# Performance work log

Measured on AMD Instinct MI355X. Metric: run time of the kernel, lower is better.

Reference implementation:

```python
import jax, jax.numpy as jnp
import numpy as np

B, L, D, M = 8, 2048, 512, 256
D2, H = 2 * D, 4 * D  # attention d_model, FFN hidden
EPS = 1e-6


def setup_inputs() -> dict:
    key = jax.random.key(0)
    ks = jax.random.split(key, 16)
    s2 = 1.0 / np.sqrt(D2)
    sD = 1.0 / np.sqrt(D)
    sH = 1.0 / np.sqrt(H)
    f32 = jnp.float32
    return {
        "zr": jax.random.normal(ks[0], (B, L, D), f32),
        "zi": jax.random.normal(ks[1], (B, L, D), f32),
        "Wq": jax.random.normal(ks[2], (D2, D2), f32) * s2,
        "Wk": jax.random.normal(ks[3], (D2, D2), f32) * s2,
        "Wv": jax.random.normal(ks[4], (D2, D2), f32) * s2,
        "Wo": jax.random.normal(ks[5], (D2, D2), f32) * s2,
        "Wf": jax.random.normal(ks[6], (M, D2), f32),  # trainable random features (std normal, FAVOR+)
        "b_attn": jnp.zeros((D,), f32),
        "W1r": jax.random.normal(ks[7], (D, H), f32) * sD,
        "W1i": jax.random.normal(ks[8], (D, H), f32) * sD,
        "b1r": jnp.zeros((H,), f32),
        "b1i": jnp.zeros((H,), f32),
        "W2r": jax.random.normal(ks[9], (H, D), f32) * sH,
        "W2i": jax.random.normal(ks[10], (H, D), f32) * sH,
        "b2r": jnp.zeros((D,), f32),
        "b2i": jnp.zeros((D,), f32),
        "b_ffn": jnp.zeros((D,), f32),
    }


def modrelu(xr, xi, b):
    # ModReLU: relu(|z| + b) * z / |z|, per-channel bias b
    mag = jnp.sqrt(xr * xr + xi * xi + EPS)
    s = jax.nn.relu(mag + b) / mag
    return xr * s, xi * s


def _block(zr, zi, Wq, Wk, Wv, Wo, Wf, b_attn,
           W1r, W1i, b1r, b1i, W2r, W2i, b2r, b2i, b_ffn):
    # --- kernelized linear attention on real/imag concat [B,L,2D] ---
    x = jnp.concatenate([zr, zi], axis=-1)
    scl = D2 ** -0.25
    q = (x @ Wq) * scl
    k = (x @ Wk) * scl
    v = x @ Wv
    # FAVOR+ positive features: phi(u) = exp(Wf u - |u|^2/2) / sqrt(m)
    pq = q @ Wf.T - 0.5 * jnp.sum(q * q, axis=-1, keepdims=True)  # [B,L,M]
    pk = k @ Wf.T - 0.5 * jnp.sum(k * k, axis=-1, keepdims=True)
    phi_q = jnp.exp(pq - jax.lax.stop_gradient(jnp.max(pq, axis=-1, keepdims=True))) / np.sqrt(M)
    phi_k = jnp.exp(pk - jax.lax.stop_gradient(jnp.max(pk))) / np.sqrt(M)
    kv = jnp.einsum('blm,bld->bmd', phi_k, v)              # [B,M,2D]
    den = jnp.einsum('blm,bm->bl', phi_q, phi_k.sum(axis=1))  # [B,L]
    y = jnp.einsum('blm,bmd->bld', phi_q, kv) / (den[..., None] + EPS)
    y = y @ Wo
    yr, yi = y[..., :D], y[..., D:]
    # Add & Norm (ModReLU)
    zr, zi = modrelu(zr + yr, zi + yi, b_attn)
    # --- complex FFN: complex Linear -> CReLU -> complex Linear ---
    hr = zr @ W1r - zi @ W1i + b1r
    hi = zr @ W1i + zi @ W1r + b1i
    hr = jax.nn.relu(hr)
    hi = jax.nn.relu(hi)
    fr = hr @ W2r - hi @ W2i + b2r
    fi = hr @ W2i + hi @ W2r + b2i
    # Add & Norm (ModReLU)
    zr, zi = modrelu(zr + fr, zi + fi, b_ffn)
    return jnp.stack([zr, zi], axis=-1)  # [B,L,D,2]


def reference(zr, zi, Wq, Wk, Wv, Wo, Wf, b_attn,
              W1r, W1i, b1r, b1i, W2r, W2i, b2r, b2i, b_ffn):
    return _block(zr, zi, Wq, Wk, Wv, Wo, Wf, b_attn,
                  W1r, W1i, b1r, b1i, W2r, W2i, b2r, b2i, b_ffn)
```

## Files before the change

### kernel.cpp

```cpp
#include <hip/hip_runtime.h>
#include <math.h>

#define B_ 8
#define L_ 2048
#define D_ 512
#define M_ 256
#define D2_ 1024
#define H_ 2048
#define N_ 16384
#define EPS_ 1e-6f

typedef __attribute__((ext_vector_type(8))) short bf16x8;
typedef __attribute__((ext_vector_type(4))) float f32x4;
typedef unsigned short ushort_t;
typedef unsigned int uint_t;

#define WAITCNT_VM8 0x0F78
#define WAITCNT_VM6 0x0F76
#define WAITCNT_VM4 0x0F74
#define WAITCNT_VM0 0x0F70

__device__ __forceinline__ ushort_t f2bf(float f) {
    uint_t u = __float_as_uint(f);
    u += 0x7FFFu + ((u >> 16) & 1u);
    return (ushort_t)(u >> 16);
}
__device__ __forceinline__ float bf2f(ushort_t u) {
    return __uint_as_float(((uint_t)u) << 16);
}
__device__ __forceinline__ void gload_lds16(const void* g, void* l) {
    __builtin_amdgcn_global_load_lds(
        (const __attribute__((address_space(1))) void*)g,
        (__attribute__((address_space(3))) void*)l, 16, 0, 0);
}

__global__ __launch_bounds__(256)
void gemm_mfma(const ushort_t* __restrict__ A, const ushort_t* __restrict__ Bm,
               void* __restrict__ Cp, int K, int lda, int ldb, int ldc,
               long long sA, long long sB, long long sC,
               int epi, float alpha, const float* __restrict__ aux,
               int auxStride, const float* __restrict__ bias, int obf)
{
    __shared__ ushort_t As[4][128 * 32];
    __shared__ ushort_t Bs[4][128 * 32];

    const int bz = blockIdx.z;
    A  += (long long)bz * sA;
    Bm += (long long)bz * sB;
    const int row0 = blockIdx.y * 128;
    const int col0 = blockIdx.x * 128;

    const int tid  = threadIdx.x;
    const int lane = tid & 63;
    const int wave = tid >> 6;
    const int wr = wave >> 1, wc = wave & 1;

    const int srow = tid >> 2;
    const int skol = (((tid & 3) ^ ((tid >> 3) & 3)) * 8);

    f32x4 acc[4][4];
    #pragma unroll
    for (int i = 0; i < 4; ++i)
        #pragma unroll
        for (int j = 0; j < 4; ++j)
            acc[i][j] = (f32x4){0.f, 0.f, 0.f, 0.f};

    const int fr = lane & 15;
    const int fq = lane >> 4;
    const int koff = ((fq ^ ((fr >> 1) & 3))) * 8;

    const int nT = K >> 5;

    auto issue = [&](int t) {
        const int buf = t & 3;
        const int k0 = t << 5;
        gload_lds16(A + (long long)(row0 + srow) * lda + k0 + skol,
                    &As[buf][(wave * 16) * 32]);
        gload_lds16(A + (long long)(row0 + 64 + srow) * lda + k0 + skol,
                    &As[buf][(64 + wave * 16) * 32]);
        gload_lds16(Bm + (long long)(col0 + srow) * ldb + k0 + skol,
                    &Bs[buf][(wave * 16) * 32]);
        gload_lds16(Bm + (long long)(col0 + 64 + srow) * ldb + k0 + skol,
                    &Bs[buf][(64 + wave * 16) * 32]);
    };

    issue(0);
    if (nT > 1) issue(1);
    for (int t = 0; t < nT; ++t) {
        if (t + 2 < nT) {
            issue(t + 2);
            __builtin_amdgcn_s_waitcnt(WAITCNT_VM8);
        } else if (t + 1 < nT) {
            __builtin_amdgcn_s_waitcnt(WAITCNT_VM4);
        } else {
            __builtin_amdgcn_s_waitcnt(WAITCNT_VM0);
        }
        __builtin_amdgcn_s_barrier();

        const int cur = t & 3;
        bf16x8 a[4], b[4];
        #pragma unroll
        for (int i = 0; i < 4; ++i)
            a[i] = *(const bf16x8*)&As[cur][(wr * 64 + i * 16 + fr) * 32 + koff];
        #pragma unroll
        for (int j = 0; j < 4; ++j)
            b[j] = *(const bf16x8*)&Bs[cur][(wc * 64 + j * 16 + fr) * 32 + koff];
        #pragma unroll
        for (int i = 0; i < 4; ++i)
            #pragma unroll
            for (int j = 0; j < 4; ++j)
                acc[i][j] = __builtin_amdgcn_mfma_f32_16x16x32_bf16(
                    a[i], b[j], acc[i][j], 0, 0, 0);
    }

    const int gr0 = row0 + wr * 64;
    const int gc0 = col0 + wc * 64;
    #pragma unroll
    for (int i = 0; i < 4; ++i) {
        #pragma unroll
        for (int r = 0; r < 4; ++r) {
            const int row = gr0 + i * 16 + fq * 4 + r;
            float raux = 0.f;
            if (epi == 1 || epi == 2) raux = aux[(long long)bz * auxStride + row];
            #pragma unroll
            for (int j = 0; j < 4; ++j) {
                const int col = gc0 + j * 16 + fr;
                float v = acc[i][j][r];
                if (epi == 0)      v *= alpha;
                else if (epi == 1) v -= 0.5f * raux;
                else if (epi == 2) v = v / (raux + EPS_);
                else if (epi == 5) v -= 0.5f * aux[(long long)bz * auxStride + col];
                else if (epi == 3) { v += bias[col]; v = v > 0.f ? v : 0.f; }
                else if (epi == 4) v += bias[col];
                const long long off = (long long)bz * sC + (long long)row * ldc + col;
                if (obf) ((ushort_t*)Cp)[off] = f2bf(v);
                else     ((float*)Cp)[off] = v;
            }
        }
    }
}

__global__ __launch_bounds__(512, 2)
void gemm256(const ushort_t* __restrict__ A, const ushort_t* __restrict__ Bm,
             void* __restrict__ Cp, int K, int lda, int ldb, int ldc,
             long long sA, long long sB, long long sC,
             int epi, float alpha, const float* __restrict__ aux,
             int auxStride, const float* __restrict__ bias, int obf)
{
    __shared__ ushort_t As[2][256 * 64];
    __shared__ ushort_t Bs[2][256 * 64];

    const int bz = blockIdx.z;
    A  += (long long)bz * sA;
    Bm += (long long)bz * sB;
    const int row0 = blockIdx.y * 256;
    const int col0 = blockIdx.x * 256;

    const int tid  = threadIdx.x;
    const int lane = tid & 63;
    const int wave = tid >> 6;
    const int wr   = wave >> 2;
    const int wcn  = wave & 3;

    const int rloc  = tid >> 3;
    const int csrc8 = (((tid & 7) ^ (rloc & 7)) << 3);

    const int fr = lane & 15;
    const int fq = lane >> 4;
    const int sw = fr & 7;
    const int c0off = ((fq ^ sw) << 3);
    const int c1off = (((4 | fq) ^ sw) << 3);

    const int nT = K >> 6;

    f32x4 acc[8][4];
    #pragma unroll
    for (int i = 0; i < 8; ++i)
        #pragma unroll
        for (int j = 0; j < 4; ++j)
            acc[i][j] = (f32x4){0.f, 0.f, 0.f, 0.f};

    bf16x8 a[4][2];
    bf16x8 b[4][2];

    auto stage = [&](int bufS, int tS, int half) {
        const int k0 = tS << 6;
        const int rh = (half >= 2) ? 1 : 0;
        const bool isA = (half == 0 || half == 3);
        const ushort_t* g = isA
            ? A  + (long long)(row0 + rh * 128 + rloc) * lda + k0 + csrc8
            : Bm + (long long)(col0 + rh * 128 + rloc) * ldb + k0 + csrc8;
        const long long gstep = 64LL * (isA ? lda : ldb);
        ushort_t* l = (isA ? &As[bufS][0] : &Bs[bufS][0])
                      + (rh * 128 + wave * 8) * 64;
        gload_lds16(g, l);
        gload_lds16(g + gstep, l + 64 * 64);
    };

    auto ldsA = [&](int buf, int mh, int i, int koff) -> bf16x8 {
        return *(const bf16x8*)
            &As[buf][(wr * 128 + mh * 64 + i * 16 + fr) * 64 + koff];
    };
    auto ldsB = [&](int buf, int j, int koff) -> bf16x8 {
        return *(const bf16x8*)
            &Bs[buf][(wcn * 64 + j * 16 + fr) * 64 + koff];
    };

    stage(0, 0, 0); stage(0, 0, 1); stage(0, 0, 2); stage(0, 0, 3);
    stage(1, 1, 0); stage(1, 1, 1); stage(1, 1, 2);
    __builtin_amdgcn_s_waitcnt(WAITCNT_VM6);
    __builtin_amdgcn_s_barrier();

    auto tile_body = [&](int t, int buf) {
        #pragma unroll
        for (int i = 0; i < 4; ++i) {
            a[i][0] = ldsA(buf, 0, i, c0off);
            a[i][1] = ldsA(buf, 0, i, c1off);
        }
        #pragma unroll
        for (int j = 0; j < 2; ++j) {
            b[j][0] = ldsB(buf, j, c0off);
            b[j][1] = ldsB(buf, j, c1off);
        }
        if (t + 1 < nT) stage(buf ^ 1, t + 1, 3);
        __builtin_amdgcn_s_barrier();
        asm volatile("s_waitcnt lgkmcnt(0)" ::: "memory");
        __builtin_amdgcn_s_setprio(1);
        #pragma unroll
        for (int i = 0; i < 4; ++i)
            #pragma unroll
            for (int j = 0; j < 2; ++j) {
                acc[i][j] = __builtin_amdgcn_mfma_f32_16x16x32_bf16(
                    a[i][0], b[j][0], acc[i][j], 0, 0, 0);
                acc[i][j] = __builtin_amdgcn_mfma_f32_16x16x32_bf16(
                    a[i][1], b[j][1], acc[i][j], 0, 0, 0);
            }
        __builtin_amdgcn_s_setprio(0);
        __builtin_amdgcn_s_barrier();

        #pragma unroll
        for (int j = 2; j < 4; ++j) {
            b[j][0] = ldsB(buf, j, c0off);
            b[j][1] = ldsB(buf, j, c1off);
        }
        __builtin_amdgcn_s_barrier();
        asm volatile("s_waitcnt lgkmcnt(0)" ::: "memory");
        __builtin_amdgcn_s_setprio(1);
        #pragma unroll
        for (int i = 0; i < 4; ++i)
            #pragma unroll
            for (int j = 2; j < 4; ++j) {
                acc[i][j] = __builtin_amdgcn_mfma_f32_16x16x32_bf16(
                    a[i][0], b[j][0], acc[i][j], 0, 0, 0);
                acc[i][j] = __builtin_amdgcn_mfma_f32_16x16x32_bf16(
                    a[i][1], b[j][1], acc[i][j], 0, 0, 0);
            }
        __builtin_amdgcn_s_setprio(0);
        __builtin_amdgcn_s_barrier();

        #pragma unroll
        for (int i = 0; i < 4; ++i) {
            a[i][0] = ldsA(buf, 1, i, c0off);
            a[i][1] = ldsA(buf, 1, i, c1off);
        }
        if (t + 2 < nT) stage(buf, t + 2, 1);
        __builtin_amdgcn_s_barrier();
        asm volatile("s_waitcnt lgkmcnt(0)" ::: "memory");
        __builtin_amdgcn_s_setprio(1);
        #pragma unroll
        for (int i = 0; i < 4; ++i)
            #pragma unroll
            for (int j = 2; j < 4; ++j) {
                acc[4 + i][j] = __builtin_amdgcn_mfma_f32_16x16x32_bf16(
                    a[i][0], b[j][0], acc[4 + i][j], 0, 0, 0);
                acc[4 + i][j] = __builtin_amdgcn_mfma_f32_16x16x32_bf16(
                    a[i][1], b[j][1], acc[4 + i][j], 0, 0, 0);
            }
        __builtin_amdgcn_s_setprio(0);
        __builtin_amdgcn_s_barrier();

        if (t + 2 < nT) { stage(buf, t + 2, 2); stage(buf, t + 2, 0); }
        __builtin_amdgcn_s_barrier();
        asm volatile("s_waitcnt lgkmcnt(0)" ::: "memory");
        __builtin_amdgcn_s_setprio(1);
        #pragma unroll
        for (int i = 0; i < 4; ++i)
            #pragma unroll
            for (int j = 0; j < 2; ++j) {
                acc[4 + i][j] = __builtin_amdgcn_mfma_f32_16x16x32_bf16(
                    a[i][0], b[j][0], acc[4 + i][j], 0, 0, 0);
                acc[4 + i][j] = __builtin_amdgcn_mfma_f32_16x16x32_bf16(
                    a[i][1], b[j][1], acc[4 + i][j], 0, 0, 0);
            }
        __builtin_amdgcn_s_setprio(0);
        if (t + 2 < nT)      __builtin_amdgcn_s_waitcnt(WAITCNT_VM6);
        else if (t + 1 < nT) __builtin_amdgcn_s_waitcnt(WAITCNT_VM0);
        __builtin_amdgcn_s_barrier();
    };

    for (int t = 0; t < nT; t += 2) {
        tile_body(t, 0);
        tile_body(t + 1, 1);
    }

    const int gr0 = row0 + wr * 128;
    const int gc0 = col0 + wcn * 64;
    #pragma unroll
    for (int i = 0; i < 8; ++i) {
        #pragma unroll
        for (int r = 0; r < 4; ++r) {
            const int row = gr0 + i * 16 + fq * 4 + r;
            float raux = 0.f;
            if (epi == 1 || epi == 2) raux = aux[(long long)bz * auxStride + row];
            #pragma unroll
            for (int j = 0; j < 4; ++j) {
                const int col = gc0 + j * 16 + fr;
                float v = acc[i][j][r];
                if (epi == 0)      v *= alpha;
                else if (epi == 1) v -= 0.5f * raux;
                else if (epi == 2) v = v / (raux + EPS_);
                else if (epi == 5) v -= 0.5f * aux[(long long)bz * auxStride + col];
                else if (epi == 3) { v += bias[col]; v = v > 0.f ? v : 0.f; }
                else if (epi == 4) v += bias[col];
                const long long off = (long long)bz * sC + (long long)row * ldc + col;
                if (obf) ((ushort_t*)Cp)[off] = f2bf(v);
                else     ((float*)Cp)[off] = v;
            }
        }
    }
}


__global__ __launch_bounds__(256)
void transpose_cvt_sq(const float* __restrict__ W, ushort_t* __restrict__ out)
{
    __shared__ float S[32][33];
    const int tx = threadIdx.x & 31, ty = threadIdx.x >> 5;
    const int n0 = blockIdx.x * 32, k0 = blockIdx.y * 32;
    #pragma unroll
    for (int r = 0; r < 4; ++r)
        S[ty + 8 * r][tx] = W[(long long)(k0 + ty + 8 * r) * 1024 + n0 + tx];
    __syncthreads();
    #pragma unroll
    for (int r = 0; r < 4; ++r)
        out[(long long)(n0 + ty + 8 * r) * 1024 + k0 + tx] = f2bf(S[tx][ty + 8 * r]);
}

__global__ __launch_bounds__(256)
void build_wc1T(const float* __restrict__ W1r, const float* __restrict__ W1i,
                ushort_t* __restrict__ out)
{
    __shared__ float S[32][33];
    const int tx = threadIdx.x & 31, ty = threadIdx.x >> 5;
    const int i0 = blockIdx.x * 32, j0 = blockIdx.y * 32;
    #pragma unroll
    for (int r = 0; r < 4; ++r) {
        const int i = i0 + ty + 8 * r, j = j0 + tx;
        float v;
        if (j < H_) v = (i < D_) ? W1r[(long long)i * H_ + j]
                                 : -W1i[(long long)(i - D_) * H_ + j];
        else {
            const int jj = j - H_;
            v = (i < D_) ? W1i[(long long)i * H_ + jj]
                         : W1r[(long long)(i - D_) * H_ + jj];
        }
        S[tx][ty + 8 * r] = v;
    }
    __syncthreads();
    #pragma unroll
    for (int r = 0; r < 4; ++r)
        out[(long long)(j0 + ty + 8 * r) * 1024 + i0 + tx] = f2bf(S[ty + 8 * r][tx]);
}

__global__ __launch_bounds__(256)
void build_wc2T(const float* __restrict__ W2r, const float* __restrict__ W2i,
                ushort_t* __restrict__ out)
{
    __shared__ float S[32][33];
    const int tx = threadIdx.x & 31, ty = threadIdx.x >> 5;
    const int i0 = blockIdx.x * 32, j0 = blockIdx.y * 32;
    #pragma unroll
    for (int r = 0; r < 4; ++r) {
        const int i = i0 + ty + 8 * r, j = j0 + tx;
        float v;
        if (i < H_) v = (j < D_) ? W2r[(long long)i * D_ + j]
                                 : W2i[(long long)i * D_ + (j - D_)];
        else {
            const int ii = i - H_;
            v = (j < D_) ? -W2i[(long long)ii * D_ + j]
                         : W2r[(long long)ii * D_ + (j - D_)];
        }
        S[tx][ty + 8 * r] = v;
    }
    __syncthreads();
    #pragma unroll
    for (int r = 0; r < 4; ++r)
        out[(long long)(j0 + ty + 8 * r) * 4096 + i0 + tx] = f2bf(S[ty + 8 * r][tx]);
}

__global__ __launch_bounds__(256)
void build_bias(const float* __restrict__ b1r, const float* __restrict__ b1i,
                const float* __restrict__ b2r, const float* __restrict__ b2i,
                float* __restrict__ bc1, float* __restrict__ bc2)
{
    const int t = blockIdx.x * 256 + threadIdx.x;
    bc1[t] = (t < H_) ? b1r[t] : b1i[t - H_];
    if (t < D2_) bc2[t] = (t < D_) ? b2r[t] : b2i[t - D_];
}

__global__ __launch_bounds__(256)
void cvt_Wf(const float* __restrict__ Wf, ushort_t* __restrict__ out)
{
    const int t = blockIdx.x * 256 + threadIdx.x;
    out[t] = f2bf(Wf[t]);
}

__global__ __launch_bounds__(256)
void cvt_x(const float* __restrict__ zr, const float* __restrict__ zi,
           ushort_t* __restrict__ x)
{
    long long t = (long long)blockIdx.x * 256 + threadIdx.x;
    long long n = t >> 8;
    int j4 = (int)(t & 255) << 2;
    float4 v;
    if (j4 < D_) v = *(const float4*)(zr + n * D_ + j4);
    else         v = *(const float4*)(zi + n * D_ + (j4 - D_));
    uint2 o;
    o.x = (uint_t)f2bf(v.x) | ((uint_t)f2bf(v.y) << 16);
    o.y = (uint_t)f2bf(v.z) | ((uint_t)f2bf(v.w) << 16);
    *(uint2*)(x + n * D2_ + j4) = o;
}

__global__ __launch_bounds__(256)
void rowsumsq_bf(const ushort_t* __restrict__ A, float* __restrict__ out)
{
    const int wid = threadIdx.x >> 6, lane = threadIdx.x & 63;
    const long long row = (long long)blockIdx.x * 4 + wid;
    const ushort_t* a = A + row * D2_;
    float s = 0.f;
    #pragma unroll
    for (int h = 0; h < 2; ++h) {
        uint4 u = *(const uint4*)(a + h * 512 + lane * 8);
        const uint_t w[4] = {u.x, u.y, u.z, u.w};
        #pragma unroll
        for (int p = 0; p < 4; ++p) {
            float lo = bf2f((ushort_t)(w[p] & 0xffff));
            float hi = bf2f((ushort_t)(w[p] >> 16));
            s += lo * lo + hi * hi;
        }
    }
    #pragma unroll
    for (int off = 32; off; off >>= 1) s += __shfl_down(s, off, 64);
    if (lane == 0) out[row] = s;
}

__global__ __launch_bounds__(256)
void phi_rowmax_exp(const float* __restrict__ P, ushort_t* __restrict__ out)
{
    const long long row = blockIdx.x;
    const int t = threadIdx.x;
    const float v = P[row * M_ + t];
    float m = v;
    #pragma unroll
    for (int off = 32; off; off >>= 1) m = fmaxf(m, __shfl_down(m, off, 64));
    __shared__ float sm[4];
    const int wid = t >> 6, lane = t & 63;
    if (lane == 0) sm[wid] = m;
    __syncthreads();
    const float mm = fmaxf(fmaxf(sm[0], sm[1]), fmaxf(sm[2], sm[3]));
    out[row * M_ + t] = f2bf(expf(v - mm) * 0.0625f);
}

__global__ __launch_bounds__(256)
void gmax1(const float* __restrict__ P, float* __restrict__ part, int n)
{
    float m = -3.4e38f;
    for (long long i = (long long)blockIdx.x * 256 + threadIdx.x; i < n;
         i += (long long)gridDim.x * 256)
        m = fmaxf(m, P[i]);
    #pragma unroll
    for (int off = 32; off; off >>= 1) m = fmaxf(m, __shfl_down(m, off, 64));
    __shared__ float sm[4];
    const int wid = threadIdx.x >> 6, lane = threadIdx.x & 63;
    if (lane == 0) sm[wid] = m;
    __syncthreads();
    if (threadIdx.x == 0)
        part[blockIdx.x] = fmaxf(fmaxf(sm[0], sm[1]), fmaxf(sm[2], sm[3]));
}

__global__ __launch_bounds__(256)
void gmax2(float* __restrict__ red)
{
    float m = -3.4e38f;
    for (int i = threadIdx.x; i < 1024; i += 256) m = fmaxf(m, red[256 + i]);
    #pragma unroll
    for (int off = 32; off; off >>= 1) m = fmaxf(m, __shfl_down(m, off, 64));
    __shared__ float sm[4];
    const int wid = threadIdx.x >> 6, lane = threadIdx.x & 63;
    if (lane == 0) sm[wid] = m;
    __syncthreads();
    if (threadIdx.x == 0) red[0] = fmaxf(fmaxf(sm[0], sm[1]), fmaxf(sm[2], sm[3]));
}

__global__ __launch_bounds__(256)
void phikT_exp(const float* __restrict__ P, const float* __restrict__ red,
               ushort_t* __restrict__ out)
{
    const long long i = (long long)blockIdx.x * 256 + threadIdx.x;
    out[i] = f2bf(expf(P[i] - red[0]) * 0.0625f);
}

__global__ __launch_bounds__(256)
void ksum_k(const ushort_t* __restrict__ phikT, float* __restrict__ ks)
{
    const int b = blockIdx.x >> 8, m = blockIdx.x & 255;
    const ushort_t* p = phikT + (long long)m * N_ + b * L_;
    uint4 u = *(const uint4*)(p + threadIdx.x * 8);
    const uint_t w[4] = {u.x, u.y, u.z, u.w};
    float s = 0.f;
    #pragma unroll
    for (int q = 0; q < 4; ++q)
        s += bf2f((ushort_t)(w[q] & 0xffff)) + bf2f((ushort_t)(w[q] >> 16));
    #pragma unroll
    for (int off = 32; off; off >>= 1) s += __shfl_down(s, off, 64);
    __shared__ float sm[4];
    const int wid = threadIdx.x >> 6, lane = threadIdx.x & 63;
    if (lane == 0) sm[wid] = s;
    __syncthreads();
    if (threadIdx.x == 0)
        ks[blockIdx.x] = sm[0] + sm[1] + sm[2] + sm[3];
}

__global__ __launch_bounds__(256)
void den_k(const ushort_t* __restrict__ phiq, const float* __restrict__ ks,
           float* __restrict__ den)
{
    const int wid = threadIdx.x >> 6, lane = threadIdx.x & 63;
    const long long n = (long long)blockIdx.x * 4 + wid;
    const int b = (int)(n >> 11);
    uint2 u = *(const uint2*)(phiq + n * M_ + lane * 4);
    float4 kk = *(const float4*)(ks + b * M_ + lane * 4);
    float s = bf2f((ushort_t)(u.x & 0xffff)) * kk.x
            + bf2f((ushort_t)(u.x >> 16)) * kk.y
            + bf2f((ushort_t)(u.y & 0xffff)) * kk.z
            + bf2f((ushort_t)(u.y >> 16)) * kk.w;
    #pragma unroll
    for (int off = 32; off; off >>= 1) s += __shfl_down(s, off, 64);
    if (lane == 0) den[n] = s;
}

__global__ __launch_bounds__(256)
void modrelu_attn(const float* __restrict__ zr, const float* __restrict__ zi,
                  const float* __restrict__ yo, const float* __restrict__ b_attn,
                  ushort_t* __restrict__ zst)
{
    const long long t = (long long)blockIdx.x * 256 + threadIdx.x;
    const long long n = t >> 9; const int d = (int)(t & 511);
    const float ar = zr[t] + yo[n * D2_ + d];
    const float ai = zi[t] + yo[n * D2_ + D_ + d];
    const float mag = sqrtf(ar * ar + ai * ai + EPS_);
    const float s = fmaxf(mag + b_attn[d], 0.f) / mag;
    zst[n * D2_ + d]      = f2bf(ar * s);
    zst[n * D2_ + D_ + d] = f2bf(ai * s);
}

__global__ __launch_bounds__(256)
void modrelu_out(const ushort_t* __restrict__ zst, const float* __restrict__ f,
                 const float* __restrict__ b_ffn, float* __restrict__ out)
{
    const long long t = (long long)blockIdx.x * 256 + threadIdx.x;
    const long long n = t >> 9; const int d = (int)(t & 511);
    const float ar = bf2f(zst[n * D2_ + d])      + f[n * D2_ + d];
    const float ai = bf2f(zst[n * D2_ + D_ + d]) + f[n * D2_ + D_ + d];
    const float mag = sqrtf(ar * ar + ai * ai + EPS_);
    const float s = fmaxf(mag + b_ffn[d], 0.f) / mag;
    out[t * 2]     = ar * s;
    out[t * 2 + 1] = ai * s;
}

extern "C" void kernel_launch(void* const* d_in, const int* in_sizes, int n_in,
                              void* d_out, int out_size, void* d_ws, size_t ws_size,
                              hipStream_t stream)
{
    const float* zr    = (const float*)d_in[0];
    const float* zi    = (const float*)d_in[1];
    const float* Wq    = (const float*)d_in[2];
    const float* Wk    = (const float*)d_in[3];
    const float* Wv    = (const float*)d_in[4];
    const float* Wo    = (const float*)d_in[5];
    const float* Wf    = (const float*)d_in[6];
    const float* b_attn= (const float*)d_in[7];
    const float* W1r   = (const float*)d_in[8];
    const float* W1i   = (const float*)d_in[9];
    const float* b1r   = (const float*)d_in[10];
    const float* b1i   = (const float*)d_in[11];
    const float* W2r   = (const float*)d_in[12];
    const float* W2i   = (const float*)d_in[13];
    const float* b2r   = (const float*)d_in[14];
    const float* b2i   = (const float*)d_in[15];
    const float* b_ffn = (const float*)d_in[16];

    char* w = (char*)d_ws;
    ushort_t* Xbf = (ushort_t*)(w + 0LL);
    ushort_t* A1  = (ushort_t*)(w + 33554432LL);
    float*    P   = (float*)   (w + 67108864LL);
    ushort_t* WqT = (ushort_t*)(w + 83886080LL);
    ushort_t* WkT = (ushort_t*)(w + 85983232LL);
    ushort_t* WvT = (ushort_t*)(w + 88080384LL);
    ushort_t* Wfb = (ushort_t*)(w + 90177536LL);
    ushort_t* F1  = (ushort_t*)(w + 100663296LL);
    ushort_t* F2  = (ushort_t*)(w + 109051904LL);
    ushort_t* WoT = (ushort_t*)(w + 117440512LL);
    ushort_t* KVT = (ushort_t*)(w + 119537664LL);
    float* ssqq = (float*)(w + 123731968LL);
    float* ssqk = (float*)(w + 123797504LL);
    float* den  = (float*)(w + 123863040LL);
    float* ksum = (float*)(w + 123928576LL);
    float* red  = (float*)(w + 123936768LL);

    const bool big = ws_size >= 152000000ULL;
    const int  RCH = big ? 8192 : 4096;
    ushort_t* Hb = (ushort_t*)(w + 33554432LL);
    float* Fb  = big ? (float*)(w + 117440512LL) : (float*)(w + 67108864LL);
    float* bc1 = big ? (float*)(w + 150994944LL) : (float*)(w + 123944960LL);
    float* bc2 = big ? (float*)(w + 151011328LL) : (float*)(w + 123961344LL);

    const float scl = 0.1767766952966369f;
    dim3 blk(256);

    auto GM = [&](const ushort_t* A, const ushort_t* Bm, void* C,
                  int rows, int cols, int K, int lda, int ldb, int ldc,
                  long long sA, long long sB, long long sC, int nb,
                  int epi, float alpha, const float* aux, int auxStride,
                  const float* bias, int obf) {
        const long long wg256 = (long long)(cols >> 8) * (rows >> 8) * nb;
        if ((rows & 255) == 0 && (cols & 255) == 0 && (K & 127) == 0 &&
            wg256 >= 128) {
            dim3 grid(cols / 256, rows / 256, nb);
            gemm256<<<grid, dim3(512), 0, stream>>>(A, Bm, C, K, lda, ldb, ldc,
                                                    sA, sB, sC, epi, alpha, aux,
                                                    auxStride, bias, obf);
        } else {
            dim3 grid(cols / 128, rows / 128, nb);
            gemm_mfma<<<grid, blk, 0, stream>>>(A, Bm, C, K, lda, ldb, ldc,
                                                sA, sB, sC, epi, alpha, aux,
                                                auxStride, bias, obf);
        }
    };

    transpose_cvt_sq<<<dim3(32, 32), blk, 0, stream>>>(Wq, WqT);
    transpose_cvt_sq<<<dim3(32, 32), blk, 0, stream>>>(Wk, WkT);
    transpose_cvt_sq<<<dim3(32, 32), blk, 0, stream>>>(Wv, WvT);
    transpose_cvt_sq<<<dim3(32, 32), blk, 0, stream>>>(Wo, WoT);
    cvt_Wf<<<1024, blk, 0, stream>>>(Wf, Wfb);
    build_bias<<<16, blk, 0, stream>>>(b1r, b1i, b2r, b2i, bc1, bc2);
    cvt_x<<<N_ * (D2_ / 4) / 256, blk, 0, stream>>>(zr, zi, Xbf);

    GM(Xbf, WqT, A1, N_, D2_, D2_, D2_, D2_, D2_, 0, 0, 0, 1, 0, scl, nullptr, 0, nullptr, 1);
    rowsumsq_bf<<<N_ / 4, blk, 0, stream>>>(A1, ssqq);
    GM(A1, Wfb, P, N_, M_, D2_, D2_, D2_, M_, 0, 0, 0, 1, 1, 1.f, ssqq, 0, nullptr, 0);
    phi_rowmax_exp<<<N_, blk, 0, stream>>>(P, F1);

    GM(Xbf, WkT, A1, N_, D2_, D2_, D2_, D2_, D2_, 0, 0, 0, 1, 0, scl, nullptr, 0, nullptr, 1);
    rowsumsq_bf<<<N_ / 4, blk, 0, stream>>>(A1, ssqk);
    GM(Wfb, A1, P, M_, N_, D2_, D2_, D2_, N_, 0, 0, 0, 1, 5, 1.f, ssqk, 0, nullptr, 0);
    gmax1<<<1024, blk, 0, stream>>>(P, red + 256, M_ * N_);
    gmax2<<<1, blk, 0, stream>>>(red);
    phikT_exp<<<M_ * N_ / 256, blk, 0, stream>>>(P, red, F2);

    GM(WvT, Xbf, A1, D2_, N_, D2_, D2_, D2_, N_, 0, 0, 0, 1, 0, 1.f, nullptr, 0, nullptr, 1);

    ksum_k<<<B_ * M_, blk, 0, stream>>>(F2, ksum);
    GM(A1, F2, KVT, D2_, M_, L_, N_, N_, M_, L_, L_, (long long)D2_ * M_, B_,
       0, 1.f, nullptr, 0, nullptr, 1);

    den_k<<<N_ / 4, blk, 0, stream>>>(F1, ksum, den);
    GM(F1, KVT, A1, L_, D2_, M_, M_, M_, D2_, (long long)L_ * M_,
       (long long)D2_ * M_, (long long)L_ * D2_, B_, 2, 1.f, den, L_, nullptr, 1);

    for (int c = 0; c < 2; ++c) {
        const long long ro = (long long)c * 8192;
        GM(A1 + ro * D2_, WoT, P, 8192, D2_, D2_, D2_, D2_, D2_, 0, 0, 0, 1,
           0, 1.f, nullptr, 0, nullptr, 0);
        modrelu_attn<<<8192 * D_ / 256, blk, 0, stream>>>(
            zr + ro * D_, zi + ro * D_, P, b_attn, Xbf + ro * D2_);
    }

    build_wc1T<<<dim3(32, 128), blk, 0, stream>>>(W1r, W1i, F1);
    build_wc2T<<<dim3(128, 32), blk, 0, stream>>>(W2r, W2i, F2);

    for (int c = 0; c < N_ / RCH; ++c) {
        const long long ro = (long long)c * RCH;
        GM(Xbf + ro * D2_, F1, Hb, RCH, 2 * H_, D2_, D2_, D2_, 2 * H_,
           0, 0, 0, 1, 3, 1.f, nullptr, 0, bc1, 1);
        GM(Hb, F2, Fb, RCH, D2_, 2 * H_, 2 * H_, 2 * H_, D2_,
           0, 0, 0, 1, 4, 1.f, nullptr, 0, bc2, 0);
        modrelu_out<<<RCH * D_ / 256, blk, 0, stream>>>(
            Xbf + ro * D2_, Fb, b_ffn, (float*)d_out + ro * D2_);
    }

    (void)in_sizes; (void)n_in; (void)out_size;
}
```

Baseline: 1.115 ms.

## Split-K the second FFN GEMM with atomic accumulation and XCD-aware block remap

```diff
diff --git a/kernel.cpp b/kernel.cpp
--- a/kernel.cpp
+++ b/kernel.cpp
@@ -145,16 +145,33 @@
              void* __restrict__ Cp, int K, int lda, int ldb, int ldc,
              long long sA, long long sB, long long sC,
              int epi, float alpha, const float* __restrict__ aux,
-             int auxStride, const float* __restrict__ bias, int obf)
+             int auxStride, const float* __restrict__ bias, int obf,
+             int ksplit)
 {
     __shared__ ushort_t As[2][256 * 64];
     __shared__ ushort_t Bs[2][256 * 64];
 
-    const int bz = blockIdx.z;
-    A  += (long long)bz * sA;
-    Bm += (long long)bz * sB;
-    const int row0 = blockIdx.y * 256;
-    const int col0 = blockIdx.x * 256;
+    const int gx = gridDim.x, gy = gridDim.y, gz = gridDim.z;
+    {
+    }
+    int fid = blockIdx.x + gx * (blockIdx.y + gy * blockIdx.z);
+    const int nwg = gx * gy * gz;
+    const int qch = nwg >> 3, rch = nwg & 7;
+    const int xcd = fid & 7, idx = fid >> 3;
+    int nid = (xcd < rch ? xcd * (qch + 1) : rch * (qch + 1) + (xcd - rch) * qch)
+              + idx;
+    const int bx = nid % gx; nid /= gx;
+    const int by = nid % gy;
+    const int bzf = nid / gy;
+
+    const int bz = bzf / ksplit;
+    const int kz = bzf - bz * ksplit;
+    const int Kh = K / ksplit;
+
+    A  += (long long)bz * sA + (long long)kz * Kh;
+    Bm += (long long)bz * sB + (long long)kz * Kh;
+    const int row0 = by * 256;
+    const int col0 = bx * 256;
 
     const int tid  = threadIdx.x;
     const int lane = tid & 63;
@@ -171,7 +188,7 @@
     const int c0off = ((fq ^ sw) << 3);
     const int c1off = (((4 | fq) ^ sw) << 3);
 
-    const int nT = K >> 6;
+    const int nT = Kh >> 6;
 
     f32x4 acc[8][4];
     #pragma unroll
@@ -316,18 +333,29 @@
             for (int j = 0; j < 4; ++j) {
                 const int col = gc0 + j * 16 + fr;
                 float v = acc[i][j][r];
+                const long long off = (long long)bz * sC + (long long)row * ldc + col;
+                if (ksplit > 1) {
+                    atomicAdd((float*)Cp + off, v * alpha);
+                    continue;
+                }
                 if (epi == 0)      v *= alpha;
                 else if (epi == 1) v -= 0.5f * raux;
                 else if (epi == 2) v = v / (raux + EPS_);
                 else if (epi == 5) v -= 0.5f * aux[(long long)bz * auxStride + col];
                 else if (epi == 3) { v += bias[col]; v = v > 0.f ? v : 0.f; }
                 else if (epi == 4) v += bias[col];
-                const long long off = (long long)bz * sC + (long long)row * ldc + col;
                 if (obf) ((ushort_t*)Cp)[off] = f2bf(v);
                 else     ((float*)Cp)[off] = v;
             }
         }
     }
+}
+
+__global__ __launch_bounds__(256)
+void seed_c(const float* __restrict__ bias, float* __restrict__ C)
+{
+    const long long t = (long long)blockIdx.x * 256 + threadIdx.x;
+    C[t] = bias ? bias[(int)(t & (D2_ - 1))] : 0.f;
 }
 
 
@@ -639,7 +667,7 @@
             dim3 grid(cols / 256, rows / 256, nb);
             gemm256<<<grid, dim3(512), 0, stream>>>(A, Bm, C, K, lda, ldb, ldc,
                                                     sA, sB, sC, epi, alpha, aux,
-                                                    auxStride, bias, obf);
+                                                    auxStride, bias, obf, 1);
         } else {
             dim3 grid(cols / 128, rows / 128, nb);
             gemm_mfma<<<grid, blk, 0, stream>>>(A, Bm, C, K, lda, ldb, ldc,
@@ -693,8 +721,16 @@
         const long long ro = (long long)c * RCH;
         GM(Xbf + ro * D2_, F1, Hb, RCH, 2 * H_, D2_, D2_, D2_, 2 * H_,
            0, 0, 0, 1, 3, 1.f, nullptr, 0, bc1, 1);
-        GM(Hb, F2, Fb, RCH, D2_, 2 * H_, 2 * H_, 2 * H_, D2_,
-           0, 0, 0, 1, 4, 1.f, nullptr, 0, bc2, 0);
+        if (RCH == 8192) {
+            seed_c<<<RCH * D2_ / 256, blk, 0, stream>>>(bc2, Fb);
+            dim3 grid2(D2_ / 256, RCH / 256, 2);
+            gemm256<<<grid2, dim3(512), 0, stream>>>(
+                Hb, F2, Fb, 2 * H_, 2 * H_, 2 * H_, D2_,
+                0, 0, 0, 4, 1.f, nullptr, 0, bc2, 0, 2);
+        } else {
+            GM(Hb, F2, Fb, RCH, D2_, 2 * H_, 2 * H_, 2 * H_, D2_,
+               0, 0, 0, 1, 4, 1.f, nullptr, 0, bc2, 0);
+        }
         modrelu_out<<<RCH * D_ / 256, blk, 0, stream>>>(
             Xbf + ro * D2_, Fb, b_ffn, (float*)d_out + ro * D2_);
     }
```

Measured after the change: 1.121 ms. No clear change (+0.5%).
